# Kernel optimization log

Measured on AMD Instinct MI355X. Metric: run time of the kernel, lower is better.

The kernel has to match this reference:

```python
import jax, jax.numpy as jnp
import numpy as np

D = 128        # feature_dims
ITERS = 2      # update_iters
B, R = 8, 256  # n segments (proteins), residues per segment
NEG_SLOPE = 0.1

def leaky(x):
    return jax.nn.leaky_relu(x, NEG_SLOPE)

def setup_inputs() -> dict:
    key = jax.random.key(0)
    ks = jax.random.split(key, 13)
    def w(k, shape):
        fan_in = shape[0]
        return jax.random.normal(k, shape, jnp.float32) / np.sqrt(fan_in)
    return {
        "fresidues": jax.random.normal(ks[0], (B, R, 20), jnp.float32),
        "coordinates": jax.random.normal(ks[1], (B, R, 3), jnp.float32) * 10.0,
        "W_emb": w(ks[2], (20, D)),                    # res_embedding (no bias)
        "W_e1": w(ks[3], (2 * D + 1, D)),              # linear_e layer 1
        "b_e1": jnp.zeros((D,), jnp.float32),
        "W_e2": w(ks[4], (D, D)),                      # linear_e layer 2
        "b_e2": jnp.zeros((D,), jnp.float32),
        "W_inf": w(ks[5], (D, 1)),                     # linear_inf gate
        "b_inf": jnp.zeros((1,), jnp.float32),
        "W_h1": w(ks[6], (2 * D, D)),                  # linear_h layer 1
        "b_h1": jnp.zeros((D,), jnp.float32),
        "W_h2": w(ks[7], (D, D)),                      # linear_h layer 2
        "b_h2": jnp.zeros((D,), jnp.float32),
    }

def reference(fresidues, coordinates, W_emb, W_e1, b_e1, W_e2, b_e2,
              W_inf, b_inf, W_h1, b_h1, W_h2, b_h2):
    # h: [B,R,D]
    h = leaky(fresidues @ W_emb)
    # pairwise squared distances: [B,R,R,1], constant across iterations
    d2 = jnp.sum(jnp.square(coordinates[:, :, None, :] - coordinates[:, None, :, :]),
                 axis=-1, keepdims=True)
    # mask out self-edges (1 - eye): [1,R,R,1]
    mask = (1.0 - jnp.eye(R, dtype=h.dtype))[None, :, :, None]
    # split edge-MLP first-layer weights to avoid materializing the [B,R,R,2D+1] concat:
    # m_input = cat([h_i, h_j, d2]) @ W_e1  ==  h_i@W_i + h_j@W_j + d2*w_d
    W_i, W_j, w_d = W_e1[:D], W_e1[D:2 * D], W_e1[2 * D]
    for _ in range(ITERS):
        ti = h @ W_i                                   # [B,R,D] receiver part
        tj = h @ W_j                                   # [B,R,D] sender part
        pre = ti[:, :, None, :] + tj[:, None, :, :] + d2 * w_d + b_e1  # [B,R,R,D]
        m = leaky(leaky(pre) @ W_e2 + b_e2)            # [B,R,R,D]
        e = jax.nn.sigmoid(m @ W_inf + b_inf) * mask   # [B,R,R,1]
        m_pre = jnp.sum(m * e, axis=2)                 # sum over senders j -> [B,R,D]
        hm = jnp.concatenate([h, m_pre], axis=-1)      # [B,R,2D]
        h = (leaky(hm @ W_h1 + b_h1) @ W_h2 + b_h2) + h
    return h

if __name__ == "__main__":
    out = reference(**setup_inputs())
    print(out.shape, out.dtype)
```

## Files before the change

### kernel.cpp

```cpp
#include <hip/hip_runtime.h>

typedef unsigned short ushort_t;
typedef __attribute__((ext_vector_type(8))) short shortx8;
typedef __attribute__((ext_vector_type(4))) float floatx4;
typedef __attribute__((ext_vector_type(2))) float floatx2;

#define NS 0.1f

__device__ __forceinline__ ushort_t f2bf_rne(float f) {
  union { float f; unsigned int u; } v; v.f = f;
  unsigned int r = v.u + 0x7FFFu + ((v.u >> 16) & 1u);
  return (ushort_t)(r >> 16);
}
__device__ __forceinline__ unsigned int pk2bf(float a, float b) {
  union { float f; unsigned int u; } x, y; x.f = a; y.f = b;
  return __builtin_amdgcn_perm(y.u + 0x8000u, x.u + 0x8000u, 0x07060302u);
}
__device__ __forceinline__ ushort_t f2bf_rhu(float f) {
  union { float f; unsigned int u; } v; v.f = f;
  return (ushort_t)((v.u + 0x8000u) >> 16);
}
__device__ __forceinline__ float lk(float x) { return fmaxf(x, NS * x); }
__device__ __forceinline__ floatx2 lk2(floatx2 v) {
  return __builtin_elementwise_max(v, v * (floatx2){NS, NS});
}

__global__ __launch_bounds__(256) void prep_w(
    const float* __restrict__ W_e1, const float* __restrict__ W_e2,
    const float* __restrict__ W_h1, const float* __restrict__ W_h2,
    ushort_t* __restrict__ wijf, ushort_t* __restrict__ we2f,
    ushort_t* __restrict__ wh1f, ushort_t* __restrict__ wh2f) {
  int e = blockIdx.x * 256 + threadIdx.x;
  int which, le;
  if (e < 32768) { which = 0; le = e; }
  else if (e < 49152) { which = 1; le = e - 32768; }
  else if (e < 81920) { which = 2; le = e - 49152; }
  else { which = 3; le = e - 81920; }
  const int NT = (which == 0) ? 16 : 8;
  int f = le >> 3, j = le & 7;
  int lane = f & 63, ft = f >> 6;
  int t = ft % NT, s = ft / NT;
  int n = t * 16 + (lane & 15), k = s * 32 + (lane >> 4) * 8 + j;
  float v; ushort_t* d;
  if (which == 0) { v = (n < 128) ? W_e1[k * 128 + n] : W_e1[(128 + k) * 128 + (n - 128)]; d = wijf; }
  else if (which == 1) { v = W_e2[k * 128 + n]; d = we2f; }
  else if (which == 2) { v = W_h1[k * 128 + n]; d = wh1f; }
  else { v = W_h2[k * 128 + n]; d = wh2f; }
  d[le] = f2bf_rne(v);
}

__device__ __forceinline__ void proj_store(float v, int m, int n,
                                           float* __restrict__ ti, float* __restrict__ tjf) {
  if (n < 128) {
    ti[(size_t)m * 128 + n] = v;
  } else {
    int k = n - 128, b = m >> 8, j = m & 255;
    int s = k >> 5, lg2 = (k >> 3) & 3, j8 = k & 7;
    tjf[((((size_t)(b * 4 + s)) * 256 + j) * 4 + lg2) * 8 + j8] = v;
  }
}

__global__ __launch_bounds__(256) void h0_proj(
    const float* __restrict__ fres, const float* __restrict__ Wemb,
    const ushort_t* __restrict__ wijf, float* __restrict__ h_out,
    float* __restrict__ ti, float* __restrict__ tjf) {
  const int m0 = blockIdx.x * 16;
  const int tid = threadIdx.x;
  const int w = tid >> 6, lane = tid & 63, l16 = lane & 15, lg = lane >> 4;
  __shared__ __align__(16) ushort_t sH[16][136];
  {
    const int row = tid >> 4, c0 = (tid & 15) * 8;
    const float* fr = fres + (size_t)(m0 + row) * 20;
    float a[8] = {0, 0, 0, 0, 0, 0, 0, 0};
    for (int k = 0; k < 20; ++k) {
      float fv = fr[k];
      float4 w0 = *(const float4*)(Wemb + k * 128 + c0);
      float4 w1 = *(const float4*)(Wemb + k * 128 + c0 + 4);
      a[0] += fv * w0.x; a[1] += fv * w0.y; a[2] += fv * w0.z; a[3] += fv * w0.w;
      a[4] += fv * w1.x; a[5] += fv * w1.y; a[6] += fv * w1.z; a[7] += fv * w1.w;
    }
#pragma unroll
    for (int x = 0; x < 8; ++x) a[x] = lk(a[x]);
    float* ho = h_out + (size_t)(m0 + row) * 128 + c0;
    *(float4*)ho = (float4){a[0], a[1], a[2], a[3]};
    *(float4*)(ho + 4) = (float4){a[4], a[5], a[6], a[7]};
    unsigned int* sh = (unsigned int*)&sH[row][c0];
    sh[0] = pk2bf(a[0], a[1]); sh[1] = pk2bf(a[2], a[3]);
    sh[2] = pk2bf(a[4], a[5]); sh[3] = pk2bf(a[6], a[7]);
  }
  __syncthreads();
  floatx4 ap[4];
#pragma unroll
  for (int q = 0; q < 4; ++q) ap[q] = (floatx4){0.f, 0.f, 0.f, 0.f};
  const shortx8* Wp = (const shortx8*)wijf;
#pragma unroll
  for (int s = 0; s < 4; ++s) {
    shortx8 af = *(const shortx8*)&sH[l16][s * 32 + lg * 8];
#pragma unroll
    for (int q = 0; q < 4; ++q)
      ap[q] = __builtin_amdgcn_mfma_f32_16x16x32_bf16(af, Wp[(s * 16 + 4 * w + q) * 64 + lane], ap[q], 0, 0, 0);
  }
#pragma unroll
  for (int q = 0; q < 4; ++q) {
    const int n = (4 * w + q) * 16 + l16;
#pragma unroll
    for (int r = 0; r < 4; ++r) proj_store(ap[q][r], m0 + lg * 4 + r, n, ti, tjf);
  }
}

__global__ __launch_bounds__(256, 3) void edge_kernel(
    const float* __restrict__ ti, const float* __restrict__ tjf,
    const float* __restrict__ coords, const ushort_t* __restrict__ we2f,
    const float* __restrict__ W_e1, const float* __restrict__ b_e1,
    const float* __restrict__ b_e2, const float* __restrict__ W_inf,
    const float* __restrict__ b_inf, float* __restrict__ mp0, float* __restrict__ mp1) {
  const int blk = blockIdx.x;
  const int b = blk >> 9, i = (blk >> 1) & 255, ch = blk & 1;
  const int tid = threadIdx.x;
  const int w = tid >> 6, lane = tid & 63, l16 = lane & 15, lg = lane >> 4;

  __shared__ __align__(16) ushort_t sW[16384];
  __shared__ __align__(16) float sTiP[128];
  __shared__ __align__(16) float sWd[128];
  __shared__ __align__(16) float sD2[128];
  __shared__ __align__(16) float sMp[4][128];

  {
    shortx8* dst = (shortx8*)sW;
    const shortx8* src = (const shortx8*)we2f;
#pragma unroll
    for (int r = 0; r < 8; ++r) dst[r * 256 + tid] = src[r * 256 + tid];
  }
  if (tid < 128) {
    sTiP[tid] = ti[(size_t)(b * 256 + i) * 128 + tid] + b_e1[tid];
    sWd[tid] = W_e1[256 * 128 + tid];
    const int j = ch * 128 + tid;
    float dx = coords[(size_t)(b * 256 + i) * 3 + 0] - coords[(size_t)(b * 256 + j) * 3 + 0];
    float dy = coords[(size_t)(b * 256 + i) * 3 + 1] - coords[(size_t)(b * 256 + j) * 3 + 1];
    float dz = coords[(size_t)(b * 256 + i) * 3 + 2] - coords[(size_t)(b * 256 + j) * 3 + 2];
    sD2[tid] = dx * dx + dy * dy + dz * dz;
  }
  floatx4 acc[2][8];
#pragma unroll
  for (int t = 0; t < 8; ++t) {
    float bv = b_e2[t * 16 + l16];
    acc[0][t] = (floatx4){bv, bv, bv, bv};
    acc[1][t] = acc[0][t];
  }
  __syncthreads();

  float d2a[2];
  d2a[0] = sD2[w * 16 + l16];
  d2a[1] = sD2[64 + w * 16 + l16];
  const shortx8* sWf = (const shortx8*)sW;

#pragma unroll
  for (int s = 0; s < 4; ++s) {
    const int k0 = s * 32 + lg * 8;
    floatx2 p2[4], w2[4];
#pragma unroll
    for (int x = 0; x < 4; ++x) {
      p2[x] = *(const floatx2*)&sTiP[k0 + 2 * x];
      w2[x] = *(const floatx2*)&sWd[k0 + 2 * x];
    }
    shortx8 af[2];
#pragma unroll
    for (int c = 0; c < 2; ++c) {
      const int jr = ch * 128 + c * 64 + w * 16 + l16;
      const float* tb = tjf + (((size_t)(b * 4 + s) * 256 + jr) * 4 + lg) * 8;
      float4 t0 = *(const float4*)tb;
      float4 t1 = *(const float4*)(tb + 4);
      const floatx2 d2v = (floatx2){d2a[c], d2a[c]};
      floatx2 pr0 = (floatx2){t0.x, t0.y} + (p2[0] + d2v * w2[0]);
      floatx2 pr1 = (floatx2){t0.z, t0.w} + (p2[1] + d2v * w2[1]);
      floatx2 pr2 = (floatx2){t1.x, t1.y} + (p2[2] + d2v * w2[2]);
      floatx2 pr3 = (floatx2){t1.z, t1.w} + (p2[3] + d2v * w2[3]);
      floatx2 l0 = lk2(pr0), l1 = lk2(pr1), l2 = lk2(pr2), l3 = lk2(pr3);
      union { shortx8 s8; unsigned int u[4]; } A;
      A.u[0] = pk2bf(l0.x, l0.y); A.u[1] = pk2bf(l1.x, l1.y);
      A.u[2] = pk2bf(l2.x, l2.y); A.u[3] = pk2bf(l3.x, l3.y);
      af[c] = A.s8;
    }
#pragma unroll
    for (int tg = 0; tg < 2; ++tg) {
      shortx8 b0 = sWf[(s * 8 + tg * 4 + 0) * 64 + lane];
      shortx8 b1 = sWf[(s * 8 + tg * 4 + 1) * 64 + lane];
      shortx8 b2 = sWf[(s * 8 + tg * 4 + 2) * 64 + lane];
      shortx8 b3 = sWf[(s * 8 + tg * 4 + 3) * 64 + lane];
#pragma unroll
      for (int c = 0; c < 2; ++c) {
        acc[c][tg * 4 + 0] = __builtin_amdgcn_mfma_f32_16x16x32_bf16(af[c], b0, acc[c][tg * 4 + 0], 0, 0, 0);
        acc[c][tg * 4 + 1] = __builtin_amdgcn_mfma_f32_16x16x32_bf16(af[c], b1, acc[c][tg * 4 + 1], 0, 0, 0);
        acc[c][tg * 4 + 2] = __builtin_amdgcn_mfma_f32_16x16x32_bf16(af[c], b2, acc[c][tg * 4 + 2], 0, 0, 0);
        acc[c][tg * 4 + 3] = __builtin_amdgcn_mfma_f32_16x16x32_bf16(af[c], b3, acc[c][tg * 4 + 3], 0, 0, 0);
      }
    }
  }

  float winfv[8], mp[8];
#pragma unroll
  for (int t = 0; t < 8; ++t) { winfv[t] = W_inf[t * 16 + l16]; mp[t] = 0.f; }
  const float binf = b_inf[0];
#pragma unroll
  for (int c = 0; c < 2; ++c) {
#pragma unroll
    for (int t = 0; t < 8; ++t) {
      floatx2 v0 = lk2((floatx2){acc[c][t][0], acc[c][t][1]});
      floatx2 v1 = lk2((floatx2){acc[c][t][2], acc[c][t][3]});
      acc[c][t][0] = v0.x; acc[c][t][1] = v0.y; acc[c][t][2] = v1.x; acc[c][t][3] = v1.y;
    }
    float p[4];
#pragma unroll
    for (int r = 0; r < 4; ++r) {
      float sum = 0.f;
#pragma unroll
      for (int t = 0; t < 8; ++t) sum += acc[c][t][r] * winfv[t];
      p[r] = sum;
    }
#pragma unroll
    for (int off = 1; off <= 8; off <<= 1)
#pragma unroll
      for (int r = 0; r < 4; ++r) p[r] += __shfl_xor(p[r], off);
#pragma unroll
    for (int r = 0; r < 4; ++r) {
      const int jg = ch * 128 + c * 64 + w * 16 + lg * 4 + r;
      float x = p[r] + binf;
      float e = __builtin_amdgcn_rcpf(1.f + __expf(-x));
      if (jg == i) e = 0.f;
#pragma unroll
      for (int t = 0; t < 8; ++t) mp[t] += acc[c][t][r] * e;
    }
  }
#pragma unroll
  for (int t = 0; t < 8; ++t) {
    mp[t] += __shfl_xor(mp[t], 16);
    mp[t] += __shfl_xor(mp[t], 32);
  }
  if (lg == 0) {
#pragma unroll
    for (int t = 0; t < 8; ++t) sMp[w][t * 16 + l16] = mp[t];
  }
  __syncthreads();
  if (tid < 128) {
    float v = sMp[0][tid] + sMp[1][tid] + sMp[2][tid] + sMp[3][tid];
    float* mpo = ch ? mp1 : mp0;
    mpo[(size_t)(b * 256 + i) * 128 + tid] = v;
  }
}

__global__ __launch_bounds__(256) void node_kernel(
    const float* __restrict__ h_in, const float* __restrict__ mp0, const float* __restrict__ mp1,
    const ushort_t* __restrict__ wh1f, const float* __restrict__ b_h1,
    const ushort_t* __restrict__ wh2f, const float* __restrict__ b_h2,
    const ushort_t* __restrict__ wijf, float* __restrict__ h_out,
    float* __restrict__ ti, float* __restrict__ tjf, const int do_proj) {
  const int m0 = blockIdx.x * 16;
  const int tid = threadIdx.x;
  const int w = tid >> 6, lane = tid & 63, l16 = lane & 15, lg = lane >> 4;
  __shared__ __align__(16) ushort_t sA[16][264];
  __shared__ __align__(16) ushort_t sU[16][136];
  __shared__ __align__(16) ushort_t sHp[16][136];

  {
    const int row = tid >> 4, c0 = (tid & 15) * 16;
    unsigned int* dst = (unsigned int*)&sA[row][c0];
    if (c0 < 128) {
      const float* src = h_in + (size_t)(m0 + row) * 128 + c0;
#pragma unroll
      for (int x = 0; x < 8; ++x) dst[x] = pk2bf(src[2 * x], src[2 * x + 1]);
    } else {
      const float* s0 = mp0 + (size_t)(m0 + row) * 128 + (c0 - 128);
      const float* s1 = mp1 + (size_t)(m0 + row) * 128 + (c0 - 128);
#pragma unroll
      for (int x = 0; x < 8; ++x)
        dst[x] = pk2bf(s0[2 * x] + s1[2 * x], s0[2 * x + 1] + s1[2 * x + 1]);
    }
  }
  __syncthreads();
  floatx4 au[2];
#pragma unroll
  for (int q = 0; q < 2; ++q) { float bv = b_h1[(2 * w + q) * 16 + l16]; au[q] = (floatx4){bv, bv, bv, bv}; }
  const shortx8* W1 = (const shortx8*)wh1f;
#pragma unroll
  for (int s = 0; s < 8; ++s) {
    shortx8 af = *(const shortx8*)&sA[l16][s * 32 + lg * 8];
#pragma unroll
    for (int q = 0; q < 2; ++q)
      au[q] = __builtin_amdgcn_mfma_f32_16x16x32_bf16(af, W1[(s * 8 + 2 * w + q) * 64 + lane], au[q], 0, 0, 0);
  }
#pragma unroll
  for (int q = 0; q < 2; ++q)
#pragma unroll
    for (int r = 0; r < 4; ++r)
      sU[lg * 4 + r][(2 * w + q) * 16 + l16] = f2bf_rhu(lk(au[q][r]));
  __syncthreads();
  floatx4 ah[2];
#pragma unroll
  for (int q = 0; q < 2; ++q) { float bv = b_h2[(2 * w + q) * 16 + l16]; ah[q] = (floatx4){bv, bv, bv, bv}; }
  const shortx8* W2 = (const shortx8*)wh2f;
#pragma unroll
  for (int s = 0; s < 4; ++s) {
    shortx8 af = *(const shortx8*)&sU[l16][s * 32 + lg * 8];
#pragma unroll
    for (int q = 0; q < 2; ++q)
      ah[q] = __builtin_amdgcn_mfma_f32_16x16x32_bf16(af, W2[(s * 8 + 2 * w + q) * 64 + lane], ah[q], 0, 0, 0);
  }
#pragma unroll
  for (int q = 0; q < 2; ++q) {
    const int n = (2 * w + q) * 16 + l16;
#pragma unroll
    for (int r = 0; r < 4; ++r) {
      const int m = m0 + lg * 4 + r;
      float v = ah[q][r] + h_in[(size_t)m * 128 + n];
      h_out[(size_t)m * 128 + n] = v;
      sHp[lg * 4 + r][n] = f2bf_rhu(v);
    }
  }
  if (!do_proj) return;
  __syncthreads();
  floatx4 ap[4];
#pragma unroll
  for (int q = 0; q < 4; ++q) ap[q] = (floatx4){0.f, 0.f, 0.f, 0.f};
  const shortx8* Wp = (const shortx8*)wijf;
#pragma unroll
  for (int s = 0; s < 4; ++s) {
    shortx8 af = *(const shortx8*)&sHp[l16][s * 32 + lg * 8];
#pragma unroll
    for (int q = 0; q < 4; ++q)
      ap[q] = __builtin_amdgcn_mfma_f32_16x16x32_bf16(af, Wp[(s * 16 + 4 * w + q) * 64 + lane], ap[q], 0, 0, 0);
  }
#pragma unroll
  for (int q = 0; q < 4; ++q) {
    const int n = (4 * w + q) * 16 + l16;
#pragma unroll
    for (int r = 0; r < 4; ++r) proj_store(ap[q][r], m0 + lg * 4 + r, n, ti, tjf);
  }
}

extern "C" void kernel_launch(void* const* d_in, const int* in_sizes, int n_in,
                              void* d_out, int out_size, void* d_ws, size_t ws_size,
                              hipStream_t stream) {
  const float* fres   = (const float*)d_in[0];
  const float* coords = (const float*)d_in[1];
  const float* W_emb  = (const float*)d_in[2];
  const float* W_e1   = (const float*)d_in[3];
  const float* b_e1   = (const float*)d_in[4];
  const float* W_e2   = (const float*)d_in[5];
  const float* b_e2   = (const float*)d_in[6];
  const float* W_inf  = (const float*)d_in[7];
  const float* b_inf  = (const float*)d_in[8];
  const float* W_h1   = (const float*)d_in[9];
  const float* b_h1   = (const float*)d_in[10];
  const float* W_h2   = (const float*)d_in[11];
  const float* b_h2   = (const float*)d_in[12];
  float* out = (float*)d_out;

  char* ws = (char*)d_ws;
  float* hA  = (float*)(ws + (0 << 20));
  float* hB  = (float*)(ws + (1 << 20));
  float* tib = (float*)(ws + (2 << 20));
  float* tjf = (float*)(ws + (3 << 20));
  float* mp0 = (float*)(ws + (4 << 20));
  float* mp1 = (float*)(ws + (5 << 20));
  ushort_t* wijf = (ushort_t*)(ws + (6 << 20));
  ushort_t* we2f = wijf + 32768;
  ushort_t* wh1f = we2f + 16384;
  ushort_t* wh2f = wh1f + 32768;

  prep_w<<<384, 256, 0, stream>>>(W_e1, W_e2, W_h1, W_h2, wijf, we2f, wh1f, wh2f);
  h0_proj<<<128, 256, 0, stream>>>(fres, W_emb, wijf, hA, tib, tjf);

  edge_kernel<<<4096, 256, 0, stream>>>(tib, tjf, coords, we2f, W_e1, b_e1, b_e2, W_inf, b_inf, mp0, mp1);
  node_kernel<<<128, 256, 0, stream>>>(hA, mp0, mp1, wh1f, b_h1, wh2f, b_h2, wijf, hB, tib, tjf, 1);

  edge_kernel<<<4096, 256, 0, stream>>>(tib, tjf, coords, we2f, W_e1, b_e1, b_e2, W_inf, b_inf, mp0, mp1);
  node_kernel<<<128, 256, 0, stream>>>(hB, mp0, mp1, wh1f, b_h1, wh2f, b_h2, wijf, out, tib, tjf, 0);
}
```

Measured before the change: 180.2 us.

## Process both sender halves per edge block to amortize W_e2 shared-memory staging

Each edge block now handles one receiver i and both 128-sender chunks in a loop, where before it handled a single chunk. The grid is halved to 2048 blocks, so the 32KB W_e2 copy into LDS and the per-receiver setup are done once per receiver instead of twice. The launch-bounds occupancy hint rises from 3 to 4 blocks per CU, and the attention-gate dot product is restructured with packed float2 FMAs. The cost is longer-running blocks with fewer of them, plus extra barriers inside the chunk loop, which may hurt latency hiding and tail balance.

```diff
diff --git a/kernel.cpp b/kernel.cpp
--- a/kernel.cpp
+++ b/kernel.cpp
@@ -31,6 +31,7 @@
     ushort_t* __restrict__ wijf, ushort_t* __restrict__ we2f,
     ushort_t* __restrict__ wh1f, ushort_t* __restrict__ wh2f) {
   int e = blockIdx.x * 256 + threadIdx.x;
+  if (e >= 98304) return;
   int which, le;
   if (e < 32768) { which = 0; le = e; }
   else if (e < 49152) { which = 1; le = e - 32768; }
@@ -50,9 +51,9 @@
 }
 
 __device__ __forceinline__ void proj_store(float v, int m, int n,
-                                           float* __restrict__ ti, float* __restrict__ tjf) {
+                                           float* __restrict__ tib, float* __restrict__ tjf) {
   if (n < 128) {
-    ti[(size_t)m * 128 + n] = v;
+    tib[(size_t)m * 128 + n] = v;
   } else {
     int k = n - 128, b = m >> 8, j = m & 255;
     int s = k >> 5, lg2 = (k >> 3) & 3, j8 = k & 7;
@@ -63,7 +64,7 @@
 __global__ __launch_bounds__(256) void h0_proj(
     const float* __restrict__ fres, const float* __restrict__ Wemb,
     const ushort_t* __restrict__ wijf, float* __restrict__ h_out,
-    float* __restrict__ ti, float* __restrict__ tjf) {
+    float* __restrict__ tib, float* __restrict__ tjf) {
   const int m0 = blockIdx.x * 16;
   const int tid = threadIdx.x;
   const int w = tid >> 6, lane = tid & 63, l16 = lane & 15, lg = lane >> 4;
@@ -104,25 +105,25 @@
   for (int q = 0; q < 4; ++q) {
     const int n = (4 * w + q) * 16 + l16;
 #pragma unroll
-    for (int r = 0; r < 4; ++r) proj_store(ap[q][r], m0 + lg * 4 + r, n, ti, tjf);
-  }
-}
-
-__global__ __launch_bounds__(256, 3) void edge_kernel(
-    const float* __restrict__ ti, const float* __restrict__ tjf,
+    for (int r = 0; r < 4; ++r) proj_store(ap[q][r], m0 + lg * 4 + r, n, tib, tjf);
+  }
+}
+
+__global__ __launch_bounds__(256, 4) void edge_kernel(
+    const float* __restrict__ tib, const float* __restrict__ tjf,
     const float* __restrict__ coords, const ushort_t* __restrict__ we2f,
     const float* __restrict__ W_e1, const float* __restrict__ b_e1,
     const float* __restrict__ b_e2, const float* __restrict__ W_inf,
     const float* __restrict__ b_inf, float* __restrict__ mp0, float* __restrict__ mp1) {
   const int blk = blockIdx.x;
-  const int b = blk >> 9, i = (blk >> 1) & 255, ch = blk & 1;
+  const int b = blk >> 8, i = blk & 255;
   const int tid = threadIdx.x;
   const int w = tid >> 6, lane = tid & 63, l16 = lane & 15, lg = lane >> 4;
 
   __shared__ __align__(16) ushort_t sW[16384];
   __shared__ __align__(16) float sTiP[128];
   __shared__ __align__(16) float sWd[128];
-  __shared__ __align__(16) float sD2[128];
+  __shared__ __align__(16) float sD2[256];
   __shared__ __align__(16) float sMp[4][128];
 
   {
@@ -132,119 +133,134 @@
     for (int r = 0; r < 8; ++r) dst[r * 256 + tid] = src[r * 256 + tid];
   }
   if (tid < 128) {
-    sTiP[tid] = ti[(size_t)(b * 256 + i) * 128 + tid] + b_e1[tid];
+    sTiP[tid] = tib[(size_t)blk * 128 + tid] + b_e1[tid];
     sWd[tid] = W_e1[256 * 128 + tid];
-    const int j = ch * 128 + tid;
+  }
+  {
+    const int j = tid;
     float dx = coords[(size_t)(b * 256 + i) * 3 + 0] - coords[(size_t)(b * 256 + j) * 3 + 0];
     float dy = coords[(size_t)(b * 256 + i) * 3 + 1] - coords[(size_t)(b * 256 + j) * 3 + 1];
     float dz = coords[(size_t)(b * 256 + i) * 3 + 2] - coords[(size_t)(b * 256 + j) * 3 + 2];
-    sD2[tid] = dx * dx + dy * dy + dz * dz;
-  }
-  floatx4 acc[2][8];
+    sD2[j] = dx * dx + dy * dy + dz * dz;
+  }
+  float bev[8], winfv[8];
 #pragma unroll
   for (int t = 0; t < 8; ++t) {
-    float bv = b_e2[t * 16 + l16];
-    acc[0][t] = (floatx4){bv, bv, bv, bv};
-    acc[1][t] = acc[0][t];
-  }
-  __syncthreads();
-
-  float d2a[2];
-  d2a[0] = sD2[w * 16 + l16];
-  d2a[1] = sD2[64 + w * 16 + l16];
+    bev[t] = b_e2[t * 16 + l16];
+    winfv[t] = W_inf[t * 16 + l16];
+  }
+  const float binf = b_inf[0];
+  __syncthreads();
+
   const shortx8* sWf = (const shortx8*)sW;
 
-#pragma unroll
-  for (int s = 0; s < 4; ++s) {
-    const int k0 = s * 32 + lg * 8;
-    floatx2 p2[4], w2[4];
-#pragma unroll
-    for (int x = 0; x < 4; ++x) {
-      p2[x] = *(const floatx2*)&sTiP[k0 + 2 * x];
-      w2[x] = *(const floatx2*)&sWd[k0 + 2 * x];
-    }
-    shortx8 af[2];
+  for (int ch = 0; ch < 2; ++ch) {
+    float d2a0 = sD2[ch * 128 + w * 16 + l16];
+    float d2a1 = sD2[ch * 128 + 64 + w * 16 + l16];
+    floatx4 acc[2][8];
+#pragma unroll
+    for (int t = 0; t < 8; ++t) {
+      acc[0][t] = (floatx4){bev[t], bev[t], bev[t], bev[t]};
+      acc[1][t] = acc[0][t];
+    }
+#pragma unroll
+    for (int s = 0; s < 4; ++s) {
+      const int k0 = s * 32 + lg * 8;
+      floatx2 p2[4], w2[4];
+#pragma unroll
+      for (int x = 0; x < 4; ++x) {
+        p2[x] = *(const floatx2*)&sTiP[k0 + 2 * x];
+        w2[x] = *(const floatx2*)&sWd[k0 + 2 * x];
+      }
+      shortx8 af[2];
+#pragma unroll
+      for (int c = 0; c < 2; ++c) {
+        const int jr = ch * 128 + c * 64 + w * 16 + l16;
+        const float* tb = tjf + (((size_t)(b * 4 + s) * 256 + jr) * 4 + lg) * 8;
+        float4 t0 = *(const float4*)tb;
+        float4 t1 = *(const float4*)(tb + 4);
+        const float d2 = c ? d2a1 : d2a0;
+        const floatx2 d2v = (floatx2){d2, d2};
+        floatx2 pr0 = (floatx2){t0.x, t0.y} + (p2[0] + d2v * w2[0]);
+        floatx2 pr1 = (floatx2){t0.z, t0.w} + (p2[1] + d2v * w2[1]);
+        floatx2 pr2 = (floatx2){t1.x, t1.y} + (p2[2] + d2v * w2[2]);
+        floatx2 pr3 = (floatx2){t1.z, t1.w} + (p2[3] + d2v * w2[3]);
+        floatx2 l0 = lk2(pr0), l1 = lk2(pr1), l2 = lk2(pr2), l3 = lk2(pr3);
+        union { shortx8 s8; unsigned int uu[4]; } A;
+        A.uu[0] = pk2bf(l0.x, l0.y); A.uu[1] = pk2bf(l1.x, l1.y);
+        A.uu[2] = pk2bf(l2.x, l2.y); A.uu[3] = pk2bf(l3.x, l3.y);
+        af[c] = A.s8;
+      }
+#pragma unroll
+      for (int tg = 0; tg < 2; ++tg) {
+        shortx8 b0 = sWf[(s * 8 + tg * 4 + 0) * 64 + lane];
+        shortx8 b1 = sWf[(s * 8 + tg * 4 + 1) * 64 + lane];
+        shortx8 b2 = sWf[(s * 8 + tg * 4 + 2) * 64 + lane];
+        shortx8 b3 = sWf[(s * 8 + tg * 4 + 3) * 64 + lane];
+#pragma unroll
+        for (int c = 0; c < 2; ++c) {
+          acc[c][tg * 4 + 0] = __builtin_amdgcn_mfma_f32_16x16x32_bf16(af[c], b0, acc[c][tg * 4 + 0], 0, 0, 0);
+          acc[c][tg * 4 + 1] = __builtin_amdgcn_mfma_f32_16x16x32_bf16(af[c], b1, acc[c][tg * 4 + 1], 0, 0, 0);
+          acc[c][tg * 4 + 2] = __builtin_amdgcn_mfma_f32_16x16x32_bf16(af[c], b2, acc[c][tg * 4 + 2], 0, 0, 0);
+          acc[c][tg * 4 + 3] = __builtin_amdgcn_mfma_f32_16x16x32_bf16(af[c], b3, acc[c][tg * 4 + 3], 0, 0, 0);
+        }
+      }
+    }
+    floatx2 mpp[8];
+#pragma unroll
+    for (int t = 0; t < 8; ++t) mpp[t] = (floatx2){0.f, 0.f};
 #pragma unroll
     for (int c = 0; c < 2; ++c) {
-      const int jr = ch * 128 + c * 64 + w * 16 + l16;
-      const float* tb = tjf + (((size_t)(b * 4 + s) * 256 + jr) * 4 + lg) * 8;
-      float4 t0 = *(const float4*)tb;
-      float4 t1 = *(const float4*)(tb + 4);
-      const floatx2 d2v = (floatx2){d2a[c], d2a[c]};
-      floatx2 pr0 = (floatx2){t0.x, t0.y} + (p2[0] + d2v * w2[0]);
-      floatx2 pr1 = (floatx2){t0.z, t0.w} + (p2[1] + d2v * w2[1]);
-      floatx2 pr2 = (floatx2){t1.x, t1.y} + (p2[2] + d2v * w2[2]);
-      floatx2 pr3 = (floatx2){t1.z, t1.w} + (p2[3] + d2v * w2[3]);
-      floatx2 l0 = lk2(pr0), l1 = lk2(pr1), l2 = lk2(pr2), l3 = lk2(pr3);
-      union { shortx8 s8; unsigned int u[4]; } A;
-      A.u[0] = pk2bf(l0.x, l0.y); A.u[1] = pk2bf(l1.x, l1.y);
-      A.u[2] = pk2bf(l2.x, l2.y); A.u[3] = pk2bf(l3.x, l3.y);
-      af[c] = A.s8;
-    }
-#pragma unroll
-    for (int tg = 0; tg < 2; ++tg) {
-      shortx8 b0 = sWf[(s * 8 + tg * 4 + 0) * 64 + lane];
-      shortx8 b1 = sWf[(s * 8 + tg * 4 + 1) * 64 + lane];
-      shortx8 b2 = sWf[(s * 8 + tg * 4 + 2) * 64 + lane];
-      shortx8 b3 = sWf[(s * 8 + tg * 4 + 3) * 64 + lane];
-#pragma unroll
-      for (int c = 0; c < 2; ++c) {
-        acc[c][tg * 4 + 0] = __builtin_amdgcn_mfma_f32_16x16x32_bf16(af[c], b0, acc[c][tg * 4 + 0], 0, 0, 0);
-        acc[c][tg * 4 + 1] = __builtin_amdgcn_mfma_f32_16x16x32_bf16(af[c], b1, acc[c][tg * 4 + 1], 0, 0, 0);
-        acc[c][tg * 4 + 2] = __builtin_amdgcn_mfma_f32_16x16x32_bf16(af[c], b2, acc[c][tg * 4 + 2], 0, 0, 0);
-        acc[c][tg * 4 + 3] = __builtin_amdgcn_mfma_f32_16x16x32_bf16(af[c], b3, acc[c][tg * 4 + 3], 0, 0, 0);
-      }
-    }
-  }
-
-  float winfv[8], mp[8];
-#pragma unroll
-  for (int t = 0; t < 8; ++t) { winfv[t] = W_inf[t * 16 + l16]; mp[t] = 0.f; }
-  const float binf = b_inf[0];
-#pragma unroll
-  for (int c = 0; c < 2; ++c) {
+#pragma unroll
+      for (int t = 0; t < 8; ++t) {
+        floatx2 v0 = lk2((floatx2){acc[c][t][0], acc[c][t][1]});
+        floatx2 v1 = lk2((floatx2){acc[c][t][2], acc[c][t][3]});
+        acc[c][t][0] = v0.x; acc[c][t][1] = v0.y; acc[c][t][2] = v1.x; acc[c][t][3] = v1.y;
+      }
+      floatx2 q01 = (floatx2){0.f, 0.f}, q23 = (floatx2){0.f, 0.f};
+#pragma unroll
+      for (int t = 0; t < 8; ++t) {
+        const floatx2 wv = (floatx2){winfv[t], winfv[t]};
+        q01 += (floatx2){acc[c][t][0], acc[c][t][1]} * wv;
+        q23 += (floatx2){acc[c][t][2], acc[c][t][3]} * wv;
+      }
+      float pp[4] = {q01.x, q01.y, q23.x, q23.y};
+#pragma unroll
+      for (int off = 1; off <= 8; off <<= 1)
+#pragma unroll
+        for (int r = 0; r < 4; ++r) pp[r] += __shfl_xor(pp[r], off);
+      float e[4];
+#pragma unroll
+      for (int r = 0; r < 4; ++r) {
+        const int jg = ch * 128 + c * 64 + w * 16 + lg * 4 + r;
+        float x = pp[r] + binf;
+        e[r] = __builtin_amdgcn_rcpf(1.f + __expf(-x));
+        if (jg == i) e[r] = 0.f;
+      }
+      const floatx2 e01 = (floatx2){e[0], e[1]}, e23 = (floatx2){e[2], e[3]};
+#pragma unroll
+      for (int t = 0; t < 8; ++t) {
+        mpp[t] += (floatx2){acc[c][t][0], acc[c][t][1]} * e01;
+        mpp[t] += (floatx2){acc[c][t][2], acc[c][t][3]} * e23;
+      }
+    }
+    float mp[8];
 #pragma unroll
     for (int t = 0; t < 8; ++t) {
-      floatx2 v0 = lk2((floatx2){acc[c][t][0], acc[c][t][1]});
-      floatx2 v1 = lk2((floatx2){acc[c][t][2], acc[c][t][3]});
-      acc[c][t][0] = v0.x; acc[c][t][1] = v0.y; acc[c][t][2] = v1.x; acc[c][t][3] = v1.y;
-    }
-    float p[4];
-#pragma unroll
-    for (int r = 0; r < 4; ++r) {
-      float sum = 0.f;
-#pragma unroll
-      for (int t = 0; t < 8; ++t) sum += acc[c][t][r] * winfv[t];
-      p[r] = sum;
-    }
-#pragma unroll
-    for (int off = 1; off <= 8; off <<= 1)
-#pragma unroll
-      for (int r = 0; r < 4; ++r) p[r] += __shfl_xor(p[r], off);
-#pragma unroll
-    for (int r = 0; r < 4; ++r) {
-      const int jg = ch * 128 + c * 64 + w * 16 + lg * 4 + r;
-      float x = p[r] + binf;
-      float e = __builtin_amdgcn_rcpf(1.f + __expf(-x));
-      if (jg == i) e = 0.f;
-#pragma unroll
-      for (int t = 0; t < 8; ++t) mp[t] += acc[c][t][r] * e;
-    }
-  }
-#pragma unroll
-  for (int t = 0; t < 8; ++t) {
-    mp[t] += __shfl_xor(mp[t], 16);
-    mp[t] += __shfl_xor(mp[t], 32);
-  }
-  if (lg == 0) {
-#pragma unroll
-    for (int t = 0; t < 8; ++t) sMp[w][t * 16 + l16] = mp[t];
-  }
-  __syncthreads();
-  if (tid < 128) {
-    float v = sMp[0][tid] + sMp[1][tid] + sMp[2][tid] + sMp[3][tid];
-    float* mpo = ch ? mp1 : mp0;
-    mpo[(size_t)(b * 256 + i) * 128 + tid] = v;
+      mp[t] = mpp[t].x + mpp[t].y;
+      mp[t] += __shfl_xor(mp[t], 16);
+      mp[t] += __shfl_xor(mp[t], 32);
+    }
+    if (lg == 0) {
+#pragma unroll
+      for (int t = 0; t < 8; ++t) sMp[w][t * 16 + l16] = mp[t];
+    }
+    __syncthreads();
+    if (tid < 128) {
+      float v = sMp[0][tid] + sMp[1][tid] + sMp[2][tid] + sMp[3][tid];
+      (ch ? mp1 : mp0)[(size_t)blk * 128 + tid] = v;
+    }
+    __syncthreads();
   }
 }
 
@@ -253,14 +269,13 @@
     const ushort_t* __restrict__ wh1f, const float* __restrict__ b_h1,
     const ushort_t* __restrict__ wh2f, const float* __restrict__ b_h2,
     const ushort_t* __restrict__ wijf, float* __restrict__ h_out,
-    float* __restrict__ ti, float* __restrict__ tjf, const int do_proj) {
+    float* __restrict__ tib, float* __restrict__ tjf, const int do_proj) {
   const int m0 = blockIdx.x * 16;
   const int tid = threadIdx.x;
   const int w = tid >> 6, lane = tid & 63, l16 = lane & 15, lg = lane >> 4;
   __shared__ __align__(16) ushort_t sA[16][264];
   __shared__ __align__(16) ushort_t sU[16][136];
   __shared__ __align__(16) ushort_t sHp[16][136];
-
   {
     const int row = tid >> 4, c0 = (tid & 15) * 16;
     unsigned int* dst = (unsigned int*)&sA[row][c0];
@@ -333,7 +348,7 @@
   for (int q = 0; q < 4; ++q) {
     const int n = (4 * w + q) * 16 + l16;
 #pragma unroll
-    for (int r = 0; r < 4; ++r) proj_store(ap[q][r], m0 + lg * 4 + r, n, ti, tjf);
+    for (int r = 0; r < 4; ++r) proj_store(ap[q][r], m0 + lg * 4 + r, n, tib, tjf);
   }
 }
 
@@ -370,9 +385,9 @@
   prep_w<<<384, 256, 0, stream>>>(W_e1, W_e2, W_h1, W_h2, wijf, we2f, wh1f, wh2f);
   h0_proj<<<128, 256, 0, stream>>>(fres, W_emb, wijf, hA, tib, tjf);
 
-  edge_kernel<<<4096, 256, 0, stream>>>(tib, tjf, coords, we2f, W_e1, b_e1, b_e2, W_inf, b_inf, mp0, mp1);
+  edge_kernel<<<2048, 256, 0, stream>>>(tib, tjf, coords, we2f, W_e1, b_e1, b_e2, W_inf, b_inf, mp0, mp1);
   node_kernel<<<128, 256, 0, stream>>>(hA, mp0, mp1, wh1f, b_h1, wh2f, b_h2, wijf, hB, tib, tjf, 1);
 
-  edge_kernel<<<4096, 256, 0, stream>>>(tib, tjf, coords, we2f, W_e1, b_e1, b_e2, W_inf, b_inf, mp0, mp1);
+  edge_kernel<<<2048, 256, 0, stream>>>(tib, tjf, coords, we2f, W_e1, b_e1, b_e2, W_inf, b_inf, mp0, mp1);
   node_kernel<<<128, 256, 0, stream>>>(hB, mp0, mp1, wh1f, b_h1, wh2f, b_h2, wijf, out, tib, tjf, 0);
 }
```

Result: slower. 235.4 us (+30.6%).
